# Kernel optimization log

Measured on AMD Instinct MI355X. Metric: run time of the kernel, lower is better.

## Reference

```python
import jax, jax.numpy as jnp
import numpy as np

NUM_USER = 200000
NUM_ITEM = 100000
DIM = 64
NUM_LAYER = 2  # hardcoded in LightGCN.__init__ (lgn_single(..., num_layer=2))
AVG_DEG = 16
N = NUM_USER + NUM_ITEM
E = N * AVG_DEG
BATCH = 16384


def setup_inputs() -> dict:
    key = jax.random.key(0)
    k = jax.random.split(key, 8)
    emb_user = jax.random.normal(k[0], (NUM_USER, DIM), jnp.float32) * 0.05
    emb_item = jax.random.normal(k[1], (NUM_ITEM, DIM), jnp.float32) * 0.05
    # COO sparse normalized adjacency: out[row] += vals * x[col]
    graph_row = jax.random.randint(k[2], (E,), 0, N, dtype=jnp.int32)
    graph_col = jax.random.randint(k[3], (E,), 0, N, dtype=jnp.int32)
    graph_vals = jax.random.uniform(k[4], (E,), jnp.float32) / AVG_DEG
    user_nodes = jax.random.randint(k[5], (BATCH,), 0, NUM_USER, dtype=jnp.int32)
    pos_item_nodes = jax.random.randint(k[6], (BATCH,), 0, NUM_ITEM, dtype=jnp.int32) + NUM_USER
    neg_item_nodes = jax.random.randint(k[7], (BATCH,), 0, NUM_ITEM, dtype=jnp.int32) + NUM_USER
    return {
        "emb_user": emb_user,
        "emb_item": emb_item,
        "graph_vals": graph_vals,
        "graph_row": graph_row,
        "graph_col": graph_col,
        "user_nodes": user_nodes,
        "pos_item_nodes": pos_item_nodes,
        "neg_item_nodes": neg_item_nodes,
    }


def _spmm(vals, row, col, x):
    # torch.sparse.mm(graph, x) with graph in COO form
    return jax.ops.segment_sum(vals[:, None] * x[col], row, num_segments=N)


def reference(emb_user, emb_item, graph_vals, graph_row, graph_col,
              user_nodes, pos_item_nodes, neg_item_nodes):
    # LGN_single.forward: concat, propagate, mean over layer stack
    all_emb = jnp.concatenate([emb_user, emb_item], axis=0)  # [N, D]
    acc = all_emb
    e = all_emb
    for _ in range(NUM_LAYER):
        e = _spmm(graph_vals, graph_row, graph_col, e)
        acc = acc + e
    light_out = acc / (NUM_LAYER + 1)  # mean of stacked embeddings
    # LightGCN.forward: gather + elementwise dot scores
    u = light_out[user_nodes]          # [B, D]
    p = light_out[pos_item_nodes]      # [B, D]
    n = light_out[neg_item_nodes]      # [B, D]
    pos_scores = jnp.sum(u * p, axis=1)
    neg_scores = jnp.sum(u * n, axis=1)
    return jnp.stack([pos_scores, neg_scores])  # [2, B]
```

## Files before the change

kernel.cpp:

```cpp
#include <hip/hip_runtime.h>

#define DIM 64
#define CHUNK 4096
#define MAXNB 2048

__device__ __forceinline__ float bf2f(unsigned short h) {
    return __uint_as_float(((unsigned int)h) << 16);
}
__device__ __forceinline__ unsigned short f2bf(float f) {
    unsigned int u = __float_as_uint(f);
    return (unsigned short)((u + 0x7FFFu + ((u >> 16) & 1u)) >> 16);
}
__device__ __forceinline__ float4 bf2f4(uint2 g) {
    float4 x;
    x.x = __uint_as_float(g.x << 16);
    x.y = __uint_as_float(g.x & 0xffff0000u);
    x.z = __uint_as_float(g.y << 16);
    x.w = __uint_as_float(g.y & 0xffff0000u);
    return x;
}

__device__ __forceinline__ int blockScan256(int v, int* sh) {
    int t = threadIdx.x;
    sh[t] = v;
    __syncthreads();
    for (int off = 1; off < 256; off <<= 1) {
        int x = (t >= off) ? sh[t - off] : 0;
        __syncthreads();
        sh[t] += x;
        __syncthreads();
    }
    return sh[t];
}


__global__ void conv_k(const float* __restrict__ a, int n, unsigned short* __restrict__ o) {
    int i = blockIdx.x * blockDim.x + threadIdx.x;
    int stride = gridDim.x * blockDim.x;
    int n8 = n >> 3;
    for (int t = i; t < n8; t += stride) {
        const float4* p = (const float4*)(a + (size_t)t * 8);
        float4 x = p[0], y = p[1];
        uint4 v;
        v.x = (unsigned)f2bf(x.x) | ((unsigned)f2bf(x.y) << 16);
        v.y = (unsigned)f2bf(x.z) | ((unsigned)f2bf(x.w) << 16);
        v.z = (unsigned)f2bf(y.x) | ((unsigned)f2bf(y.y) << 16);
        v.w = (unsigned)f2bf(y.z) | ((unsigned)f2bf(y.w) << 16);
        ((uint4*)o)[t] = v;
    }
    for (int t = n8 * 8 + i; t < n; t += stride) o[t] = f2bf(a[t]);
}


__global__ void p1a_hist(const int* __restrict__ row, int E, int NB,
                         int* __restrict__ counts) {
    __shared__ int h[MAXNB];
    for (int b = threadIdx.x; b < NB; b += 256) h[b] = 0;
    __syncthreads();
    int base = blockIdx.x * CHUNK;
    int end = min(base + CHUNK, E);
    int vend = base + ((end - base) & ~3);
    for (int i = base + threadIdx.x * 4; i < vend; i += 1024) {
        int4 r = *(const int4*)(row + i);
        atomicAdd(&h[r.x >> 8], 1);
        atomicAdd(&h[r.y >> 8], 1);
        atomicAdd(&h[r.z >> 8], 1);
        atomicAdd(&h[r.w >> 8], 1);
    }
    for (int i = vend + threadIdx.x; i < end; i += 256) atomicAdd(&h[row[i] >> 8], 1);
    __syncthreads();
    int blk = blockIdx.x;
    for (int b = threadIdx.x; b < NB; b += 256) counts[(size_t)blk * NB + b] = h[b];
}

__global__ void p1b_scan(int* __restrict__ counts, int NBLK, int NB,
                         int* __restrict__ bucketTotal) {
    int b = blockIdx.x, t = threadIdx.x;
    __shared__ int sh[256];
    int v[8];
    int run = 0;
#pragma unroll
    for (int i = 0; i < 8; i++) {
        int idx = t * 8 + i;
        int c = (idx < NBLK) ? counts[(size_t)idx * NB + b] : 0;
        v[i] = run;
        run += c;
    }
    int inc = blockScan256(run, sh);
    int excl = inc - run;
#pragma unroll
    for (int i = 0; i < 8; i++) {
        int idx = t * 8 + i;
        if (idx < NBLK) counts[(size_t)idx * NB + b] = v[i] + excl;
    }
    if (t == 255) bucketTotal[b] = sh[255];
}

__global__ void p_scan_tot(const int* __restrict__ bucketTotal, int NB,
                           int* __restrict__ bucketStart) {
    int t = threadIdx.x;
    __shared__ int sh[256];
    int v[8];
    int run = 0;
#pragma unroll
    for (int i = 0; i < 8; i++) {
        int idx = t * 8 + i;
        int c = (idx < NB) ? bucketTotal[idx] : 0;
        v[i] = run;
        run += c;
    }
    int inc = blockScan256(run, sh);
    int excl = inc - run;
#pragma unroll
    for (int i = 0; i < 8; i++) {
        int idx = t * 8 + i;
        if (idx < NB) bucketStart[idx] = v[i] + excl;
    }
    if (t == 255) bucketStart[NB] = sh[255];
}

__global__ void p1c_scatter(const int* __restrict__ row, const int* __restrict__ col,
                            const float* __restrict__ vals, int E, int NB,
                            const int* __restrict__ counts, const int* __restrict__ bucketStart,
                            int2* __restrict__ bdata) {
    __shared__ int cur[MAXNB];
    int blk = blockIdx.x;
    for (int b = threadIdx.x; b < NB; b += 256)
        cur[b] = bucketStart[b] + counts[(size_t)blk * NB + b];
    __syncthreads();
    int base = blk * CHUNK;
    int end = min(base + CHUNK, E);
    int vend = base + ((end - base) & ~3);
    for (int i = base + threadIdx.x * 4; i < vend; i += 1024) {
        int4 r = *(const int4*)(row + i);
        int4 c = *(const int4*)(col + i);
        float4 v = *(const float4*)(vals + i);
        int p0 = atomicAdd(&cur[r.x >> 8], 1);
        bdata[p0] = make_int2(((r.x & 255) << 20) | c.x, __float_as_int(v.x));
        int p1 = atomicAdd(&cur[r.y >> 8], 1);
        bdata[p1] = make_int2(((r.y & 255) << 20) | c.y, __float_as_int(v.y));
        int p2 = atomicAdd(&cur[r.z >> 8], 1);
        bdata[p2] = make_int2(((r.z & 255) << 20) | c.z, __float_as_int(v.z));
        int p3 = atomicAdd(&cur[r.w >> 8], 1);
        bdata[p3] = make_int2(((r.w & 255) << 20) | c.w, __float_as_int(v.w));
    }
    for (int i = vend + threadIdx.x; i < end; i += 256) {
        int r = row[i];
        int p = atomicAdd(&cur[r >> 8], 1);
        bdata[p] = make_int2(((r & 255) << 20) | col[i], __float_as_int(vals[i]));
    }
}

__global__ void p2_group(const int2* __restrict__ bdata, const int* __restrict__ bucketStart,
                         int NB, int N, int E,
                         int* __restrict__ rowptr, int2* __restrict__ pairs) {
    __shared__ int hist[256];
    __shared__ int sh[256];
    __shared__ int cur[256];
    int b = blockIdx.x, t = threadIdx.x;
    int s0 = bucketStart[b], s1 = bucketStart[b + 1];
    hist[t] = 0;
    __syncthreads();
    for (int i = s0 + t; i < s1; i += 256)
        atomicAdd(&hist[(bdata[i].x >> 20) & 255], 1);
    __syncthreads();
    int h = hist[t];
    int inc = blockScan256(h, sh);
    int excl = inc - h;
    int r = b * 256 + t;
    if (r < N) rowptr[r] = s0 + excl;
    cur[t] = excl;
    __syncthreads();
    for (int i = s0 + t; i < s1; i += 256) {
        int2 e = bdata[i];
        int rl = (e.x >> 20) & 255;
        int pos = atomicAdd(&cur[rl], 1);
        pairs[(size_t)s0 + pos] = make_int2(e.x & 0xFFFFF, e.y);
    }
    if (b == NB - 1 && t == 0) rowptr[N] = E;
}


__global__ void spmm1_k(const unsigned short* __restrict__ emb16,
                        const int* __restrict__ rowptr, const int2* __restrict__ pairs,
                        int n_total, unsigned short* __restrict__ e1) {
    int wave = (blockIdx.x * blockDim.x + threadIdx.x) >> 6;
    int lane = threadIdx.x & 63;
    if (wave >= n_total) return;
    int eg = lane >> 4, dp = lane & 15;
    int k0 = rowptr[wave], k1 = rowptr[wave + 1];
    float4 a0 = {0.f, 0.f, 0.f, 0.f}, a1 = {0.f, 0.f, 0.f, 0.f};
    for (int k = k0; k < k1; k += 8) {
        int kk0 = k + eg;
        int kk1 = k + 4 + eg;
        int kc0 = kk0 < k1 ? kk0 : k1 - 1;
        int kc1 = kk1 < k1 ? kk1 : k1 - 1;
        int2 p0 = pairs[kc0];
        int2 p1 = pairs[kc1];
        float v0 = kk0 < k1 ? __int_as_float(p0.y) : 0.f;
        float v1 = kk1 < k1 ? __int_as_float(p1.y) : 0.f;
        uint2 g0 = *(const uint2*)(emb16 + (size_t)p0.x * DIM + dp * 4);
        uint2 g1 = *(const uint2*)(emb16 + (size_t)p1.x * DIM + dp * 4);
        float4 x0 = bf2f4(g0);
        float4 x1 = bf2f4(g1);
        a0.x += v0 * x0.x; a0.y += v0 * x0.y; a0.z += v0 * x0.z; a0.w += v0 * x0.w;
        a1.x += v1 * x1.x; a1.y += v1 * x1.y; a1.z += v1 * x1.z; a1.w += v1 * x1.w;
    }
    float4 s;
    s.x = a0.x + a1.x; s.y = a0.y + a1.y; s.z = a0.z + a1.z; s.w = a0.w + a1.w;
    s.x += __shfl_xor(s.x, 16); s.y += __shfl_xor(s.y, 16);
    s.z += __shfl_xor(s.z, 16); s.w += __shfl_xor(s.w, 16);
    s.x += __shfl_xor(s.x, 32); s.y += __shfl_xor(s.y, 32);
    s.z += __shfl_xor(s.z, 32); s.w += __shfl_xor(s.w, 32);
    if (eg == 0) {
        uint2 o;
        o.x = (unsigned)f2bf(s.x) | ((unsigned)f2bf(s.y) << 16);
        o.y = (unsigned)f2bf(s.z) | ((unsigned)f2bf(s.w) << 16);
        *(uint2*)(e1 + (size_t)wave * DIM + dp * 4) = o;
    }
}


__global__ void final_k(const float* __restrict__ emb_user, const float* __restrict__ emb_item,
                        int n_user, const unsigned short* __restrict__ e1,
                        const int* __restrict__ rowptr, const int2* __restrict__ pairs,
                        const int* __restrict__ u_nodes, const int* __restrict__ p_nodes,
                        const int* __restrict__ n_nodes, int B, float* __restrict__ out) {
    int wave = (blockIdx.x * blockDim.x + threadIdx.x) >> 6;
    int lane = threadIdx.x & 63;
    if (wave >= B) return;
    int eg = lane >> 4, dp = lane & 15;
    int nid[3] = {u_nodes[wave], p_nodes[wave], n_nodes[wave]};
    float4 l[3];
#pragma unroll
    for (int j = 0; j < 3; j++) {
        int r = nid[j];
        const float* base0 = (r < n_user) ? (emb_user + (size_t)r * DIM)
                                          : (emb_item + (size_t)(r - n_user) * DIM);
        float4 acc = *(const float4*)(base0 + dp * 4);
        float4 t1 = bf2f4(*(const uint2*)(e1 + (size_t)r * DIM + dp * 4));
        acc.x += t1.x; acc.y += t1.y; acc.z += t1.z; acc.w += t1.w;
        int k0 = rowptr[r], k1 = rowptr[r + 1];
        float4 a0 = {0.f, 0.f, 0.f, 0.f}, a1 = {0.f, 0.f, 0.f, 0.f};
        for (int k = k0; k < k1; k += 8) {
            int kk0 = k + eg;
            int kk1 = k + 4 + eg;
            int kc0 = kk0 < k1 ? kk0 : k1 - 1;
            int kc1 = kk1 < k1 ? kk1 : k1 - 1;
            int2 p0 = pairs[kc0];
            int2 p1 = pairs[kc1];
            float v0 = kk0 < k1 ? __int_as_float(p0.y) : 0.f;
            float v1 = kk1 < k1 ? __int_as_float(p1.y) : 0.f;
            uint2 g0 = *(const uint2*)(e1 + (size_t)p0.x * DIM + dp * 4);
            uint2 g1 = *(const uint2*)(e1 + (size_t)p1.x * DIM + dp * 4);
            float4 x0 = bf2f4(g0);
            float4 x1 = bf2f4(g1);
            a0.x += v0 * x0.x; a0.y += v0 * x0.y; a0.z += v0 * x0.z; a0.w += v0 * x0.w;
            a1.x += v1 * x1.x; a1.y += v1 * x1.y; a1.z += v1 * x1.z; a1.w += v1 * x1.w;
        }
        float4 s;
        s.x = a0.x + a1.x; s.y = a0.y + a1.y; s.z = a0.z + a1.z; s.w = a0.w + a1.w;
        s.x += __shfl_xor(s.x, 16); s.y += __shfl_xor(s.y, 16);
        s.z += __shfl_xor(s.z, 16); s.w += __shfl_xor(s.w, 16);
        s.x += __shfl_xor(s.x, 32); s.y += __shfl_xor(s.y, 32);
        s.z += __shfl_xor(s.z, 32); s.w += __shfl_xor(s.w, 32);
        l[j].x = (acc.x + s.x) * (1.0f / 3.0f);
        l[j].y = (acc.y + s.y) * (1.0f / 3.0f);
        l[j].z = (acc.z + s.z) * (1.0f / 3.0f);
        l[j].w = (acc.w + s.w) * (1.0f / 3.0f);
    }
    float ps = l[0].x * l[1].x + l[0].y * l[1].y + l[0].z * l[1].z + l[0].w * l[1].w;
    float ns = l[0].x * l[2].x + l[0].y * l[2].y + l[0].z * l[2].z + l[0].w * l[2].w;
    ps += __shfl_xor(ps, 1); ns += __shfl_xor(ns, 1);
    ps += __shfl_xor(ps, 2); ns += __shfl_xor(ns, 2);
    ps += __shfl_xor(ps, 4); ns += __shfl_xor(ns, 4);
    ps += __shfl_xor(ps, 8); ns += __shfl_xor(ns, 8);
    if (lane == 0) {
        out[wave] = ps;
        out[B + wave] = ns;
    }
}

extern "C" void kernel_launch(void* const* d_in, const int* in_sizes, int n_in,
                              void* d_out, int out_size, void* d_ws, size_t ws_size,
                              hipStream_t stream) {
    const float* emb_user = (const float*)d_in[0];
    const float* emb_item = (const float*)d_in[1];
    const float* gvals    = (const float*)d_in[2];
    const int*   grow     = (const int*)d_in[3];
    const int*   gcol     = (const int*)d_in[4];
    const int*   unodes   = (const int*)d_in[5];
    const int*   pnodes   = (const int*)d_in[6];
    const int*   nnodes   = (const int*)d_in[7];
    float* out = (float*)d_out;

    int n_user = in_sizes[0] / DIM;
    int n_item = in_sizes[1] / DIM;
    int N = n_user + n_item;
    int E = in_sizes[2];
    int B = in_sizes[5];
    int NB = (N + 255) >> 8;
    int NBLK = (E + CHUNK - 1) / CHUNK;

    char* ws = (char*)d_ws;
    size_t off = 0;
    auto alloc = [&](size_t bytes) -> void* {
        void* p = ws + off;
        off = (off + bytes + 255) & ~(size_t)255;
        return p;
    };
    int*  rowptr      = (int*)alloc((size_t)(N + 1) * 4);
    int*  bucketTotal = (int*)alloc((size_t)MAXNB * 4);
    int*  bucketStart = (int*)alloc((size_t)(MAXNB + 1) * 4);
    int2* pairs       = (int2*)alloc((size_t)E * 8);
    char* regionB = (char*)alloc((size_t)E * 8 > (size_t)N * DIM * 2 ? (size_t)E * 8
                                                                     : (size_t)N * DIM * 2);
    int2*           bdata = (int2*)regionB;
    unsigned short* emb16 = (unsigned short*)regionB;
    size_t countsBytes = (size_t)NBLK * NB * 4;
    size_t e1Bytes = (size_t)N * DIM * 2;
    char* regionA = (char*)alloc(countsBytes > e1Bytes ? countsBytes : e1Bytes);
    int*            counts = (int*)regionA;
    unsigned short* e1     = (unsigned short*)regionA;
    (void)ws_size; (void)n_in; (void)out_size;

    p1a_hist<<<NBLK, 256, 0, stream>>>(grow, E, NB, counts);
    p1b_scan<<<NB, 256, 0, stream>>>(counts, NBLK, NB, bucketTotal);
    p_scan_tot<<<1, 256, 0, stream>>>(bucketTotal, NB, bucketStart);
    p1c_scatter<<<NBLK, 256, 0, stream>>>(grow, gcol, gvals, E, NB, counts, bucketStart, bdata);
    p2_group<<<NB, 256, 0, stream>>>(bdata, bucketStart, NB, N, E, rowptr, pairs);

    conv_k<<<2048, 256, 0, stream>>>(emb_user, n_user * DIM, emb16);
    conv_k<<<2048, 256, 0, stream>>>(emb_item, n_item * DIM, emb16 + (size_t)n_user * DIM);

    spmm1_k<<<(N + 3) / 4, 256, 0, stream>>>(emb16, rowptr, pairs, N, e1);
    final_k<<<(B + 3) / 4, 256, 0, stream>>>(emb_user, emb_item, n_user, e1,
                                             rowptr, pairs,
                                             unodes, pnodes, nnodes, B, out);
}
```

Baseline: 320.2 us.

## Pad CSR rows to multiples of eight and stage grouping in LDS

Each row's edge list is padded to a multiple of 8 with zero-weight entries, and the edge list is stored as start/length arrays, so the SpMM inner loops drop bounds clamping and masking. Column indices are pre-shifted into byte offsets. p2_group builds each bucket in shared memory before writing it out with coalesced stores. The two bf16 conversion kernels are merged into one launch, and the scatter atomics are reordered ahead of their stores. Padding adds extra work and memory, and large buckets fall back to direct global writes.

```diff
diff --git a/kernel.cpp b/kernel.cpp
--- a/kernel.cpp
+++ b/kernel.cpp
@@ -3,10 +3,9 @@
 #define DIM 64
 #define CHUNK 4096
 #define MAXNB 2048
-
-__device__ __forceinline__ float bf2f(unsigned short h) {
-    return __uint_as_float(((unsigned int)h) << 16);
-}
+#define PADSLOP 1792
+#define P2CAP 7680
+
 __device__ __forceinline__ unsigned short f2bf(float f) {
     unsigned int u = __float_as_uint(f);
     return (unsigned short)((u + 0x7FFFu + ((u >> 16) & 1u)) >> 16);
@@ -34,13 +33,16 @@
 }
 
 
-__global__ void conv_k(const float* __restrict__ a, int n, unsigned short* __restrict__ o) {
+__global__ void conv2_k(const float* __restrict__ u, const float* __restrict__ it,
+                        int nu, int ntot, unsigned short* __restrict__ o) {
     int i = blockIdx.x * blockDim.x + threadIdx.x;
     int stride = gridDim.x * blockDim.x;
-    int n8 = n >> 3;
+    int n8 = ntot >> 3;
     for (int t = i; t < n8; t += stride) {
-        const float4* p = (const float4*)(a + (size_t)t * 8);
-        float4 x = p[0], y = p[1];
+        int e = t * 8;
+        const float* src = (e < nu) ? (u + e) : (it + (e - nu));
+        float4 x = *(const float4*)src;
+        float4 y = *(const float4*)(src + 4);
         uint4 v;
         v.x = (unsigned)f2bf(x.x) | ((unsigned)f2bf(x.y) << 16);
         v.y = (unsigned)f2bf(x.z) | ((unsigned)f2bf(x.w) << 16);
@@ -48,7 +50,6 @@
         v.w = (unsigned)f2bf(y.z) | ((unsigned)f2bf(y.w) << 16);
         ((uint4*)o)[t] = v;
     }
-    for (int t = n8 * 8 + i; t < n; t += stride) o[t] = f2bf(a[t]);
 }
 
 
@@ -136,12 +137,12 @@
         int4 c = *(const int4*)(col + i);
         float4 v = *(const float4*)(vals + i);
         int p0 = atomicAdd(&cur[r.x >> 8], 1);
+        int p1 = atomicAdd(&cur[r.y >> 8], 1);
+        int p2 = atomicAdd(&cur[r.z >> 8], 1);
+        int p3 = atomicAdd(&cur[r.w >> 8], 1);
         bdata[p0] = make_int2(((r.x & 255) << 20) | c.x, __float_as_int(v.x));
-        int p1 = atomicAdd(&cur[r.y >> 8], 1);
         bdata[p1] = make_int2(((r.y & 255) << 20) | c.y, __float_as_int(v.y));
-        int p2 = atomicAdd(&cur[r.z >> 8], 1);
         bdata[p2] = make_int2(((r.z & 255) << 20) | c.z, __float_as_int(v.z));
-        int p3 = atomicAdd(&cur[r.w >> 8], 1);
         bdata[p3] = make_int2(((r.w & 255) << 20) | c.w, __float_as_int(v.w));
     }
     for (int i = vend + threadIdx.x; i < end; i += 256) {
@@ -152,55 +153,77 @@
 }
 
 __global__ void p2_group(const int2* __restrict__ bdata, const int* __restrict__ bucketStart,
-                         int NB, int N, int E,
-                         int* __restrict__ rowptr, int2* __restrict__ pairs) {
+                         int NB, int N,
+                         int* __restrict__ rowStart, int* __restrict__ rowLen,
+                         int2* __restrict__ pairs) {
     __shared__ int hist[256];
     __shared__ int sh[256];
     __shared__ int cur[256];
+    __shared__ int2 stage[P2CAP];
     int b = blockIdx.x, t = threadIdx.x;
     int s0 = bucketStart[b], s1 = bucketStart[b + 1];
+    int pbase = s0 + b * PADSLOP;
     hist[t] = 0;
     __syncthreads();
     for (int i = s0 + t; i < s1; i += 256)
         atomicAdd(&hist[(bdata[i].x >> 20) & 255], 1);
     __syncthreads();
     int h = hist[t];
-    int inc = blockScan256(h, sh);
-    int excl = inc - h;
+    int hp = (h + 7) & ~7;
+    int inc = blockScan256(hp, sh);
+    int excl = inc - hp;
+    int ptot = sh[255];
     int r = b * 256 + t;
-    if (r < N) rowptr[r] = s0 + excl;
+    if (r < N) {
+        rowStart[r] = pbase + excl;
+        rowLen[r] = hp;
+    }
     cur[t] = excl;
     __syncthreads();
-    for (int i = s0 + t; i < s1; i += 256) {
-        int2 e = bdata[i];
-        int rl = (e.x >> 20) & 255;
-        int pos = atomicAdd(&cur[rl], 1);
-        pairs[(size_t)s0 + pos] = make_int2(e.x & 0xFFFFF, e.y);
-    }
-    if (b == NB - 1 && t == 0) rowptr[N] = E;
+    if (ptot <= P2CAP) {
+        for (int i = t; i < ptot; i += 256) stage[i] = make_int2(0, 0);
+        __syncthreads();
+        for (int i = s0 + t; i < s1; i += 256) {
+            int2 e = bdata[i];
+            int rl = (e.x >> 20) & 255;
+            int pos = atomicAdd(&cur[rl], 1);
+            stage[pos] = make_int2((e.x & 0xFFFFF) << 7, e.y);
+        }
+        __syncthreads();
+        for (int i = t; i < ptot; i += 256) pairs[pbase + i] = stage[i];
+    } else {
+        for (int i = t; i < ptot; i += 256) pairs[pbase + i] = make_int2(0, 0);
+        __syncthreads();
+        for (int i = s0 + t; i < s1; i += 256) {
+            int2 e = bdata[i];
+            int rl = (e.x >> 20) & 255;
+            int pos = atomicAdd(&cur[rl], 1);
+            pairs[pbase + pos] = make_int2((e.x & 0xFFFFF) << 7, e.y);
+        }
+    }
 }
 
 
 __global__ void spmm1_k(const unsigned short* __restrict__ emb16,
-                        const int* __restrict__ rowptr, const int2* __restrict__ pairs,
+                        const int* __restrict__ rowStart, const int* __restrict__ rowLen,
+                        const int2* __restrict__ pairs,
                         int n_total, unsigned short* __restrict__ e1) {
     int wave = (blockIdx.x * blockDim.x + threadIdx.x) >> 6;
     int lane = threadIdx.x & 63;
     if (wave >= n_total) return;
     int eg = lane >> 4, dp = lane & 15;
-    int k0 = rowptr[wave], k1 = rowptr[wave + 1];
+    unsigned off0 = dp * 8u;
+    const char* base = (const char*)emb16;
+    int len = rowLen[wave];
+    const int2* pp = pairs + rowStart[wave];
     float4 a0 = {0.f, 0.f, 0.f, 0.f}, a1 = {0.f, 0.f, 0.f, 0.f};
-    for (int k = k0; k < k1; k += 8) {
-        int kk0 = k + eg;
-        int kk1 = k + 4 + eg;
-        int kc0 = kk0 < k1 ? kk0 : k1 - 1;
-        int kc1 = kk1 < k1 ? kk1 : k1 - 1;
-        int2 p0 = pairs[kc0];
-        int2 p1 = pairs[kc1];
-        float v0 = kk0 < k1 ? __int_as_float(p0.y) : 0.f;
-        float v1 = kk1 < k1 ? __int_as_float(p1.y) : 0.f;
-        uint2 g0 = *(const uint2*)(emb16 + (size_t)p0.x * DIM + dp * 4);
-        uint2 g1 = *(const uint2*)(emb16 + (size_t)p1.x * DIM + dp * 4);
+    for (int k = 0; k < len; k += 8) {
+        int2 p0 = pp[k + eg];
+        int2 p1 = pp[k + 4 + eg];
+        uint2 g0 = *(const uint2*)(base + ((unsigned)p0.x + off0));
+        uint2 g1 = *(const uint2*)(base + ((unsigned)p1.x + off0));
+        float v0 = __int_as_float(p0.y);
+        float v1 = __int_as_float(p1.y);
         float4 x0 = bf2f4(g0);
         float4 x1 = bf2f4(g1);
         a0.x += v0 * x0.x; a0.y += v0 * x0.y; a0.z += v0 * x0.z; a0.w += v0 * x0.w;
@@ -223,13 +246,16 @@
 
 __global__ void final_k(const float* __restrict__ emb_user, const float* __restrict__ emb_item,
                         int n_user, const unsigned short* __restrict__ e1,
-                        const int* __restrict__ rowptr, const int2* __restrict__ pairs,
+                        const int* __restrict__ rowStart, const int* __restrict__ rowLen,
+                        const int2* __restrict__ pairs,
                         const int* __restrict__ u_nodes, const int* __restrict__ p_nodes,
                         const int* __restrict__ n_nodes, int B, float* __restrict__ out) {
     int wave = (blockIdx.x * blockDim.x + threadIdx.x) >> 6;
     int lane = threadIdx.x & 63;
     if (wave >= B) return;
     int eg = lane >> 4, dp = lane & 15;
+    unsigned off0 = dp * 8u;
+    const char* base = (const char*)e1;
     int nid[3] = {u_nodes[wave], p_nodes[wave], n_nodes[wave]};
     float4 l[3];
 #pragma unroll
@@ -240,19 +266,16 @@
         float4 acc = *(const float4*)(base0 + dp * 4);
         float4 t1 = bf2f4(*(const uint2*)(e1 + (size_t)r * DIM + dp * 4));
         acc.x += t1.x; acc.y += t1.y; acc.z += t1.z; acc.w += t1.w;
-        int k0 = rowptr[r], k1 = rowptr[r + 1];
+        int len = rowLen[r];
+        const int2* pp = pairs + rowStart[r];
         float4 a0 = {0.f, 0.f, 0.f, 0.f}, a1 = {0.f, 0.f, 0.f, 0.f};
-        for (int k = k0; k < k1; k += 8) {
-            int kk0 = k + eg;
-            int kk1 = k + 4 + eg;
-            int kc0 = kk0 < k1 ? kk0 : k1 - 1;
-            int kc1 = kk1 < k1 ? kk1 : k1 - 1;
-            int2 p0 = pairs[kc0];
-            int2 p1 = pairs[kc1];
-            float v0 = kk0 < k1 ? __int_as_float(p0.y) : 0.f;
-            float v1 = kk1 < k1 ? __int_as_float(p1.y) : 0.f;
-            uint2 g0 = *(const uint2*)(e1 + (size_t)p0.x * DIM + dp * 4);
-            uint2 g1 = *(const uint2*)(e1 + (size_t)p1.x * DIM + dp * 4);
+        for (int k = 0; k < len; k += 8) {
+            int2 p0 = pp[k + eg];
+            int2 p1 = pp[k + 4 + eg];
+            uint2 g0 = *(const uint2*)(base + ((unsigned)p0.x + off0));
+            uint2 g1 = *(const uint2*)(base + ((unsigned)p1.x + off0));
+            float v0 = __int_as_float(p0.y);
+            float v1 = __int_as_float(p1.y);
             float4 x0 = bf2f4(g0);
             float4 x1 = bf2f4(g1);
             a0.x += v0 * x0.x; a0.y += v0 * x0.y; a0.z += v0 * x0.z; a0.w += v0 * x0.w;
@@ -309,10 +332,11 @@
         off = (off + bytes + 255) & ~(size_t)255;
         return p;
     };
-    int*  rowptr      = (int*)alloc((size_t)(N + 1) * 4);
+    int*  rowStart    = (int*)alloc((size_t)N * 4);
+    int*  rowLen      = (int*)alloc((size_t)N * 4);
     int*  bucketTotal = (int*)alloc((size_t)MAXNB * 4);
     int*  bucketStart = (int*)alloc((size_t)(MAXNB + 1) * 4);
-    int2* pairs       = (int2*)alloc((size_t)E * 8);
+    int2* pairs       = (int2*)alloc(((size_t)E + (size_t)NB * PADSLOP) * 8);
     char* regionB = (char*)alloc((size_t)E * 8 > (size_t)N * DIM * 2 ? (size_t)E * 8
                                                                      : (size_t)N * DIM * 2);
     int2*           bdata = (int2*)regionB;
@@ -328,13 +352,12 @@
     p1b_scan<<<NB, 256, 0, stream>>>(counts, NBLK, NB, bucketTotal);
     p_scan_tot<<<1, 256, 0, stream>>>(bucketTotal, NB, bucketStart);
     p1c_scatter<<<NBLK, 256, 0, stream>>>(grow, gcol, gvals, E, NB, counts, bucketStart, bdata);
-    p2_group<<<NB, 256, 0, stream>>>(bdata, bucketStart, NB, N, E, rowptr, pairs);
-
-    conv_k<<<2048, 256, 0, stream>>>(emb_user, n_user * DIM, emb16);
-    conv_k<<<2048, 256, 0, stream>>>(emb_item, n_item * DIM, emb16 + (size_t)n_user * DIM);
-
-    spmm1_k<<<(N + 3) / 4, 256, 0, stream>>>(emb16, rowptr, pairs, N, e1);
+    p2_group<<<NB, 256, 0, stream>>>(bdata, bucketStart, NB, N, rowStart, rowLen, pairs);
+
+    conv2_k<<<2048, 256, 0, stream>>>(emb_user, emb_item, n_user * DIM, N * DIM, emb16);
+
+    spmm1_k<<<(N + 3) / 4, 256, 0, stream>>>(emb16, rowStart, rowLen, pairs, N, e1);
     final_k<<<(B + 3) / 4, 256, 0, stream>>>(emb_user, emb_item, n_user, e1,
-                                             rowptr, pairs,
+                                             rowStart, rowLen, pairs,
                                              unodes, pnodes, nnodes, B, out);
 }
```

After: 313.9 us. -2.0%, faster.
